# Optimization experiments

Hardware: AMD Instinct MI355X
Metric: run time of the kernel (lower is better)

Reference implementation:

```python
import jax, jax.numpy as jnp
import numpy as np
import math

B, L, D = 4, 2048, 128
DEGREE = 2
EPS = 1e-12  # F.normalize eps

# upper-triangular index pairs (i <= j), matching torch.triu_indices(D, D)
_TRIU_I, _TRIU_J = np.triu_indices(D)
TRIU_I = jnp.asarray(_TRIU_I)
TRIU_J = jnp.asarray(_TRIU_J)


def setup_inputs() -> dict:
    key = jax.random.key(0)
    k1, _ = jax.random.split(key)
    x = jax.random.normal(k1, (B, L, D), dtype=jnp.float32)
    degree_scales = jnp.ones((DEGREE,), dtype=jnp.float32) / math.sqrt(DEGREE)
    return {"x": x, "degree_scales": degree_scales}


def reference(x, degree_scales):
    # F.normalize(x, dim=-1): x / max(||x||_2, eps)
    norm = jnp.linalg.norm(x, axis=-1, keepdims=True)
    x_norm = x / jnp.maximum(norm, EPS)
    # degree-1 features (unscaled, matching the torch code)
    feats1 = x_norm
    # degree-2 features: only the needed upper-triangular products, no D^2 materialization
    deg2 = x_norm[..., TRIU_I] * x_norm[..., TRIU_J]  # (B, L, D*(D+1)/2)
    deg2 = deg2 * degree_scales[1]
    return jnp.concatenate([feats1, deg2], axis=-1)  # (B, L, D + D*(D+1)/2)
```

## Files before the change

### kernel.cpp

```cpp
#include <hip/hip_runtime.h>


#define DD 128
#define ROW_OUT (DD + DD * (DD + 1) / 2)
#define NCHUNK (ROW_OUT / 4)

__global__ __launch_bounds__(256) void poly_kernel(
    const float* __restrict__ x, const float* __restrict__ scales,
    float* __restrict__ out) {
  __shared__ float s_x[DD];
  __shared__ float s_c1;
  __shared__ float s_c2;

  const int row = blockIdx.x;
  const int tid = threadIdx.x;
  const float* xr = x + (size_t)row * DD;

  float partial = 0.0f;
  if (tid < 32) {
    float4 xv = ((const float4*)xr)[tid];
    ((float4*)s_x)[tid] = xv;
    partial = xv.x * xv.x + xv.y * xv.y + xv.z * xv.z + xv.w * xv.w;
  }
  if (tid < 64) {
#pragma unroll
    for (int off = 16; off >= 1; off >>= 1)
      partial += __shfl_down(partial, off, 64);
    if (tid == 0) {
      float nrm = sqrtf(partial);
      float inv = 1.0f / fmaxf(nrm, 1e-12f);
      s_c1 = inv;
      s_c2 = inv * inv * scales[1];
    }
  }
  __syncthreads();

  const float c1 = s_c1;
  const float c2 = s_c2;
  float* orow = out + (size_t)row * ROW_OUT;

  for (int p4 = tid; p4 < NCHUNK; p4 += 256) {
    const int p = p4 * 4;
    float4 v;
    if (p < DD) {
      float4 xv = ((const float4*)s_x)[p4];
      v = make_float4(xv.x * c1, xv.y * c1, xv.z * c1, xv.w * c1);
    } else {
      int k = p - DD;
      float r = sqrtf((float)(257 * 257 - 8 * k));
      int i = (int)((257.0f - r) * 0.5f);
      int off = (i * (257 - i)) >> 1;
      if (off > k) {
        --i;
        off = (i * (257 - i)) >> 1;
      } else {
        int off2 = ((i + 1) * (256 - i)) >> 1;
        if (off2 <= k) {
          ++i;
          off = off2;
        }
      }
      int j = i + (k - off);
      float xi = s_x[i] * c2;
      float vv[4];
#pragma unroll
      for (int e = 0; e < 4; ++e) {
        if (j >= DD) {
          ++i;
          j = i;
          xi = s_x[i] * c2;
        }
        vv[e] = xi * s_x[j];
        ++j;
      }
      v = make_float4(vv[0], vv[1], vv[2], vv[3]);
    }
    ((float4*)orow)[p4] = v;
  }
}

extern "C" void kernel_launch(void* const* d_in, const int* in_sizes, int n_in,
                              void* d_out, int out_size, void* d_ws,
                              size_t ws_size, hipStream_t stream) {
  const float* x = (const float*)d_in[0];
  const float* scales = (const float*)d_in[1];
  float* out = (float*)d_out;
  const int n_rows = in_sizes[0] / DD;
  poly_kernel<<<n_rows, 256, 0, stream>>>(x, scales, out);
}
```

Before: 276.0 us.

## Process four rows per block, reusing triangular index math and swizzling shared memory

```diff
diff --git a/kernel.cpp b/kernel.cpp
--- a/kernel.cpp
+++ b/kernel.cpp
@@ -4,78 +4,84 @@
 #define DD 128
 #define ROW_OUT (DD + DD * (DD + 1) / 2)
 #define NCHUNK (ROW_OUT / 4)
+#define RPB 4
 
 __global__ __launch_bounds__(256) void poly_kernel(
     const float* __restrict__ x, const float* __restrict__ scales,
     float* __restrict__ out) {
-  __shared__ float s_x[DD];
-  __shared__ float s_c1;
-  __shared__ float s_c2;
+  __shared__ __attribute__((aligned(16))) float s_plain[RPB][DD];
+  __shared__ float s_xi[RPB][DD];
+  __shared__ float s_xt[RPB][DD];
 
-  const int row = blockIdx.x;
   const int tid = threadIdx.x;
-  const float* xr = x + (size_t)row * DD;
+  const int w = tid >> 6;
+  const int l = tid & 63;
+  const int row0 = blockIdx.x * RPB;
+  const float s2 = scales[1];
 
-  float partial = 0.0f;
-  if (tid < 32) {
-    float4 xv = ((const float4*)xr)[tid];
-    ((float4*)s_x)[tid] = xv;
-    partial = xv.x * xv.x + xv.y * xv.y + xv.z * xv.z + xv.w * xv.w;
-  }
-  if (tid < 64) {
+  {
+    const float2 v = ((const float2*)(x + (size_t)(row0 + w) * DD))[l];
+    float p = v.x * v.x + v.y * v.y;
 #pragma unroll
-    for (int off = 16; off >= 1; off >>= 1)
-      partial += __shfl_down(partial, off, 64);
-    if (tid == 0) {
-      float nrm = sqrtf(partial);
-      float inv = 1.0f / fmaxf(nrm, 1e-12f);
-      s_c1 = inv;
-      s_c2 = inv * inv * scales[1];
-    }
+    for (int off = 32; off >= 1; off >>= 1) p += __shfl_xor(p, off, 64);
+    const float inv = 1.0f / fmaxf(sqrtf(p), 1e-12f);
+    const float a = v.x * inv, b = v.y * inv;
+    const int m0 = 2 * l, m1 = 2 * l + 1;
+    s_plain[w][m0] = a;
+    s_plain[w][m1] = b;
+    s_xi[w][m0] = a * s2;
+    s_xi[w][m1] = b * s2;
+    s_xt[w][((m0 & 3) << 5) + (m0 >> 2)] = a;
+    s_xt[w][((m1 & 3) << 5) + (m1 >> 2)] = b;
   }
   __syncthreads();
 
-  const float c1 = s_c1;
-  const float c2 = s_c2;
-  float* orow = out + (size_t)row * ROW_OUT;
+  float* __restrict__ o0 = out + (size_t)row0 * ROW_OUT;
 
   for (int p4 = tid; p4 < NCHUNK; p4 += 256) {
     const int p = p4 * 4;
-    float4 v;
     if (p < DD) {
-      float4 xv = ((const float4*)s_x)[p4];
-      v = make_float4(xv.x * c1, xv.y * c1, xv.z * c1, xv.w * c1);
+#pragma unroll
+      for (int r = 0; r < RPB; ++r)
+        ((float4*)(o0 + (size_t)r * ROW_OUT))[p4] =
+            ((const float4*)s_plain[r])[p4];
     } else {
-      int k = p - DD;
-      float r = sqrtf((float)(257 * 257 - 8 * k));
-      int i = (int)((257.0f - r) * 0.5f);
+      const int k = p - DD;
+      const float rr = sqrtf((float)(257 * 257 - 8 * k));
+      int i = (int)((257.0f - rr) * 0.5f);
       int off = (i * (257 - i)) >> 1;
       if (off > k) {
         --i;
         off = (i * (257 - i)) >> 1;
       } else {
-        int off2 = ((i + 1) * (256 - i)) >> 1;
+        const int off2 = ((i + 1) * (256 - i)) >> 1;
         if (off2 <= k) {
           ++i;
           off = off2;
         }
       }
       int j = i + (k - off);
-      float xi = s_x[i] * c2;
-      float vv[4];
+      int ixi[4], ixt[4];
 #pragma unroll
       for (int e = 0; e < 4; ++e) {
         if (j >= DD) {
           ++i;
           j = i;
-          xi = s_x[i] * c2;
         }
-        vv[e] = xi * s_x[j];
+        ixi[e] = i;
+        ixt[e] = ((j & 3) << 5) + (j >> 2);
         ++j;
       }
-      v = make_float4(vv[0], vv[1], vv[2], vv[3]);
+#pragma unroll
+      for (int r = 0; r < RPB; ++r) {
+        float4 v;
+        v.x = s_xi[r][ixi[0]] * s_xt[r][ixt[0]];
+        v.y = s_xi[r][ixi[1]] * s_xt[r][ixt[1]];
+        v.z = s_xi[r][ixi[2]] * s_xt[r][ixt[2]];
+        v.w = s_xi[r][ixi[3]] * s_xt[r][ixt[3]];
+        ((float4*)(o0 + (size_t)r * ROW_OUT))[p4] = v;
+      }
     }
-    ((float4*)orow)[p4] = v;
   }
 }
 
@@ -86,5 +92,5 @@
   const float* scales = (const float*)d_in[1];
   float* out = (float*)d_out;
   const int n_rows = in_sizes[0] / DD;
-  poly_kernel<<<n_rows, 256, 0, stream>>>(x, scales, out);
+  poly_kernel<<<n_rows / RPB, 256, 0, stream>>>(x, scales, out);
 }
```

Measured after the change: 274.5 us. About the same (-0.5%).
